# Optimization experiments

Measured on AMD Instinct MI355X. Metric: run time of the kernel, lower is better.

The kernel has to match this reference:

```python
import jax, jax.numpy as jnp
import numpy as np

B, NR, NF, NH, NFH, D, HID = 32, 32, 128, 64, 64, 32, 256


def setup_inputs() -> dict:
    key = jax.random.key(0)
    ks = jax.random.split(key, 16)

    def w(k, o, i):
        return (jax.random.normal(k, (o, i), jnp.float32) / np.sqrt(i)).astype(jnp.float32)

    inp = {
        "robot": jax.random.normal(ks[0], (B, NR, D), jnp.float32),
        "frontier": jax.random.normal(ks[1], (B, NF, D), jnp.float32),
        "robot_history": jax.random.normal(ks[2], (B, NH, D), jnp.float32),
        "frontier_history": jax.random.normal(ks[3], (B, NFH, D), jnp.float32),
        "robot_frontier": jax.random.uniform(ks[4], (B, NR, NF), jnp.float32),
        "robot_past": jax.random.uniform(ks[5], (B, NR, NH), jnp.float32),
        "frontier_past": jax.random.uniform(ks[6], (B, NF, NFH), jnp.float32),
        # parameters (torch Linear convention: weight [out, in])
        "Wq": w(ks[7], D, D), "bq": jnp.zeros(D, jnp.float32),
        "Wk": w(ks[8], D, D), "bk": jnp.zeros(D, jnp.float32),
        "Wv": w(ks[9], D, D), "bv": jnp.zeros(D, jnp.float32),
        "Wn1": w(ks[10], HID, 2 * D), "bn1": jnp.zeros(HID, jnp.float32),
        "Wn2": w(ks[11], D, HID), "bn2": jnp.zeros(D, jnp.float32),
        "We1": w(ks[12], HID, 2 * D + 1), "be1": jnp.zeros(HID, jnp.float32),
        "We2": w(ks[13], 1, HID), "be2": jnp.zeros(1, jnp.float32),
    }
    return inp


def reference(robot, frontier, robot_history, frontier_history, robot_frontier,
              robot_past, frontier_past, Wq, bq, Wk, bk, Wv, bv,
              Wn1, bn1, Wn2, bn2, We1, be1, We2, be2):
    def lin(x, W, b):
        return x @ W.T + b

    def nmlp(h):
        return lin(jax.nn.relu(lin(h, Wn1, bn1)), Wn2, bn2)

    def emlp(h):
        return lin(jax.nn.relu(lin(h, We1, be1)), We2, be2)

    def intra(x):  # x: [b, n, D]
        q, k, v = lin(x, Wq, bq), lin(x, Wk, bk), lin(x, Wv, bv)
        e = jax.nn.softmax(jnp.einsum('bnd,bmd->bnm', q, k), axis=-1)
        agg = jnp.einsum('bnm,bmd->bnd', e, v)
        return x + nmlp(jnp.concatenate([x, agg], axis=-1))

    def inter(x, y, dis):  # x: [b,Nx,D], y: [b,Ny,D], dis: [b,Nx,Ny]
        xq, yk, yv = lin(x, Wq, bq), lin(y, Wk, bk), lin(y, Wv, bv)
        b, Nx, _ = x.shape
        Ny = y.shape[1]
        r_i = jnp.broadcast_to(xq[:, :, None, :], (b, Nx, Ny, D))
        f_j = jnp.broadcast_to(yk[:, None, :, :], (b, Nx, Ny, D))
        edge_input = jnp.concatenate([r_i, f_j, dis[..., None]], axis=-1)  # [b,Nx,Ny,65]
        score = emlp(edge_input)[..., 0]                                   # [b,Nx,Ny]
        e = jax.nn.softmax(score, axis=-1)
        agg = jnp.einsum('bnm,bmd->bnd', e, yv)
        x = x + nmlp(jnp.concatenate([x, agg], axis=-1))
        return e, x

    robot = intra(robot)
    frontier = intra(frontier)           # == per-sample intra on [1,Nf,D]
    robot_history = intra(robot_history)
    frontier_history = intra(frontier_history)
    _, robot = inter(robot, robot_history, robot_past)
    _, new_frontier = inter(frontier, frontier_history, frontier_past)
    edge, robot = inter(robot, new_frontier, robot_frontier)
    # original returns the intra-transformed frontier (split_frontier), not new_frontier
    return (robot, frontier, robot_history, frontier_history, edge)
```

## Files before the change

### kernel.cpp

```cpp
#include <hip/hip_runtime.h>

#define BATCH 32
#define NRr 32
#define NFf 128
#define NHh 64
#define NFHh 64
#define TI 4

__device__ __forceinline__ float dot4(float4 a, float4 b) {
    return fmaf(a.x, b.x, fmaf(a.y, b.y, fmaf(a.z, b.z, a.w * b.w)));
}

__global__ __launch_bounds__(256, 4) void intra_kernel(
    const float* __restrict__ robot, const float* __restrict__ frontier,
    const float* __restrict__ rhist, const float* __restrict__ fhist,
    const float* __restrict__ Wq, const float* __restrict__ bq,
    const float* __restrict__ Wk, const float* __restrict__ bk,
    const float* __restrict__ Wv, const float* __restrict__ bv,
    const float* __restrict__ Wn1, const float* __restrict__ bn1,
    const float* __restrict__ Wn2, const float* __restrict__ bn2,
    float* __restrict__ o_robot, float* __restrict__ o_frontier,
    float* __restrict__ o_rh, float* __restrict__ o_fh)
{
    __shared__ __align__(16) float sXc[512];
    __shared__ __align__(16) float sQ[512];
    __shared__ __align__(16) float sQK[512];
    __shared__ __align__(16) float sAgg[512];
    __shared__ __align__(16) float sBig[6240];
    float* sS  = sBig;
    float* sXT = sBig + 2112;
    float* sT  = sBig;

    const int blk = blockIdx.x, tid = threadIdx.x;
    const float* xin; float* xout; int N, lgN, b, chunk;
    if (blk < 64)       { xin=robot;    xout=o_robot;    N=32;  lgN=5; b=blk>>1;       chunk=blk&1; }
    else if (blk < 320) { xin=frontier; xout=o_frontier; N=128; lgN=7; b=(blk-64)>>3;  chunk=(blk-64)&7; }
    else if (blk < 448) { xin=rhist;    xout=o_rh;       N=64;  lgN=6; b=(blk-320)>>2; chunk=(blk-320)&3; }
    else                { xin=fhist;    xout=o_fh;       N=64;  lgN=6; b=(blk-448)>>2; chunk=(blk-448)&3; }

    const int P = N + 4, P2 = N + 1;
    const float* xb = xin + (size_t)b * N * 32;
    const int r0 = chunk << 4;
    const int d = tid & 31;
    const int rloc = tid >> 5;

    sXc[tid] = xb[(r0 << 5) + tid];
    sXc[tid + 256] = xb[(r0 << 5) + tid + 256];
    for (int idx = tid; idx < (N << 5); idx += 256) {
        int j = idx >> 5, d2 = idx & 31;
        sXT[d2 * P2 + j] = xb[idx];
    }
    __syncthreads();

    {
        const float4* wq4 = (const float4*)(Wq + (d << 5));
        float4 wq[8];
        #pragma unroll
        for (int k = 0; k < 8; ++k) wq[k] = wq4[k];
        const float bqd = bq[d];
        #pragma unroll
        for (int p = 0; p < 2; ++p) {
            int rr = rloc + (p << 3);
            const float4* xr = (const float4*)(sXc + (rr << 5));
            float a = bqd;
            #pragma unroll
            for (int k = 0; k < 8; ++k) a += dot4(wq[k], xr[k]);
            sQ[(rr << 5) + d] = a;
        }
    }
    __syncthreads();

    {
        #pragma unroll
        for (int p = 0; p < 2; ++p) {
            int rr = rloc + (p << 3);
            const float* qr = sQ + (rr << 5);
            float a = 0.f;
            #pragma unroll
            for (int dd2 = 0; dd2 < 32; ++dd2)
                a = fmaf(Wk[dd2 * 32 + d], qr[dd2], a);
            sQK[(rr << 5) + d] = a;
        }
    }
    __syncthreads();

    for (int idx = tid; idx < (16 << lgN); idx += 256) {
        int r = idx >> lgN, j = idx & (N - 1);
        const float* qr = sQK + (r << 5);
        float a = 0.f;
        #pragma unroll
        for (int e = 0; e < 32; ++e) a = fmaf(qr[e], sXT[e * P2 + j], a);
        sS[r * P + j] = a;
    }
    __syncthreads();

    {
        #pragma unroll
        for (int p = 0; p < 2; ++p) {
            int rr = rloc + (p << 3);
            float* row = sS + rr * P;
            float m = -1e30f;
            for (int j = d; j < N; j += 32) m = fmaxf(m, row[j]);
            #pragma unroll
            for (int msk = 16; msk; msk >>= 1) m = fmaxf(m, __shfl_xor(m, msk));
            float s = 0.f;
            for (int j = d; j < N; j += 32) { float ev = __expf(row[j] - m); row[j] = ev; s += ev; }
            #pragma unroll
            for (int msk = 16; msk; msk >>= 1) s += __shfl_xor(s, msk);
            float inv = 1.0f / s;
            for (int j = d; j < N; j += 32) row[j] *= inv;
        }
    }
    __syncthreads();

    {
        #pragma unroll
        for (int p = 0; p < 2; ++p) {
            int rr = rloc + (p << 3);
            const float* er = sS + rr * P;
            const float* xtr = sXT + d * P2;
            float a = 0.f;
            for (int j = 0; j < N; ++j) a = fmaf(er[j], xtr[j], a);
            sQ[(rr << 5) + d] = a;
        }
    }
    __syncthreads();

    {
        const float4* wv4 = (const float4*)(Wv + (d << 5));
        float4 wv[8];
        #pragma unroll
        for (int k = 0; k < 8; ++k) wv[k] = wv4[k];
        const float bvd = bv[d];
        #pragma unroll
        for (int p = 0; p < 2; ++p) {
            int rr = rloc + (p << 3);
            const float4* zr = (const float4*)(sQ + (rr << 5));
            float a = bvd;
            #pragma unroll
            for (int k = 0; k < 8; ++k) a += dot4(wv[k], zr[k]);
            sAgg[(rr << 5) + d] = a;
        }
    }
    __syncthreads();

    {
        const float4* w14 = (const float4*)(Wn1 + (tid << 6));
        float4 w1r[16];
        #pragma unroll
        for (int k = 0; k < 16; ++k) w1r[k] = w14[k];
        const float b1 = bn1[tid];
        #pragma unroll
        for (int r = 0; r < 16; ++r) {
            const float4* xr = (const float4*)(sXc + (r << 5));
            const float4* ar = (const float4*)(sAgg + (r << 5));
            float a = b1;
            #pragma unroll
            for (int k = 0; k < 8; ++k) a += dot4(w1r[k], xr[k]);
            #pragma unroll
            for (int k = 0; k < 8; ++k) a += dot4(w1r[8 + k], ar[k]);
            sT[(r << 8) + tid] = fmaxf(a, 0.f);
        }
    }
    __syncthreads();

    {
        const int rg = tid >> 5;
        float acc0 = 0.f, acc1 = 0.f;
        #pragma unroll
        for (int hc = 0; hc < 4; ++hc) {
            const float4* w24 = (const float4*)(Wn2 + (d << 8) + (hc << 6));
            float4 w2r[16];
            #pragma unroll
            for (int k = 0; k < 16; ++k) w2r[k] = w24[k];
            const float4* t0 = (const float4*)(sT + (rg << 8) + (hc << 6));
            const float4* t1 = (const float4*)(sT + ((rg + 8) << 8) + (hc << 6));
            #pragma unroll
            for (int k = 0; k < 16; ++k) {
                acc0 += dot4(w2r[k], t0[k]);
                acc1 += dot4(w2r[k], t1[k]);
            }
        }
        const float b2 = bn2[d];
        const size_t base = ((size_t)b * N) << 5;
        xout[base + ((r0 + rg) << 5) + d]     = sXc[(rg << 5) + d] + b2 + acc0;
        xout[base + ((r0 + rg + 8) << 5) + d] = sXc[((rg + 8) << 5) + d] + b2 + acc1;
    }
}

__global__ __launch_bounds__(256) void pre_y_kernel(
    const float* __restrict__ yA, int NyA, float* __restrict__ wOutA, float* __restrict__ yvOutA, int nBlkA,
    const float* __restrict__ yB, int NyB, float* __restrict__ wOutB, float* __restrict__ yvOutB,
    int ghBase,
    const float* __restrict__ Wq, const float* __restrict__ bq,
    const float* __restrict__ Wk, const float* __restrict__ bk,
    const float* __restrict__ Wv, const float* __restrict__ bv,
    const float* __restrict__ We1, const float* __restrict__ be1,
    float* __restrict__ Gm, float* __restrict__ gvec,
    float* __restrict__ Hm, float* __restrict__ hbvec)
{
    __shared__ __align__(16) float sY[256], sK[256];
    const int blk = blockIdx.x, tid = threadIdx.x;

    if (blk >= ghBase) {
        const int hr = ((blk - ghBase) << 3) + (tid >> 5), e = tid & 31;
        const float* w1q = We1 + hr * 65;
        const float* w1k = w1q + 32;
        float aG = 0.f, aH = 0.f;
        #pragma unroll
        for (int d2 = 0; d2 < 32; ++d2) {
            aG = fmaf(w1q[d2], Wq[d2 * 32 + e], aG);
            aH = fmaf(w1k[d2], Wk[d2 * 32 + e], aH);
        }
        Gm[(hr << 5) + e] = aG;
        Hm[(hr << 5) + e] = aH;
        if (e == 0) {
            float ag = be1[hr], ahb = 0.f;
            #pragma unroll
            for (int d2 = 0; d2 < 32; ++d2) {
                ag  = fmaf(w1q[d2], bq[d2], ag);
                ahb = fmaf(w1k[d2], bk[d2], ahb);
            }
            gvec[hr] = ag;
            hbvec[hr] = ahb;
        }
        return;
    }

    const float* y; int Ny; float* wOut; float* yvOut; int idx;
    if (blk < nBlkA) { y=yA; Ny=NyA; wOut=wOutA; yvOut=yvOutA; idx=blk; }
    else             { y=yB; Ny=NyB; wOut=wOutB; yvOut=yvOutB; idx=blk-nBlkA; }
    const int chunks = Ny >> 3;
    const int b = idx / chunks, j0 = (idx - b * chunks) << 3;

    sY[tid] = y[((size_t)(b * Ny + j0)) * 32 + tid];
    __syncthreads();

    {
        int jl = tid >> 5, dd = tid & 31;
        const float4* wk4 = (const float4*)(Wk + (dd << 5));
        const float4* wv4 = (const float4*)(Wv + (dd << 5));
        const float4* yr = (const float4*)(sY + (jl << 5));
        float aK = bk[dd], aV = bv[dd];
        #pragma unroll
        for (int k = 0; k < 8; ++k) {
            float4 yv4 = yr[k];
            aK += dot4(wk4[k], yv4);
            aV += dot4(wv4[k], yv4);
        }
        sK[(jl << 5) + dd] = aK;
        yvOut[((size_t)(b * Ny + j0 + jl)) * 32 + dd] = aV;
    }
    __syncthreads();

    {
        const float* w1 = We1 + tid * 65 + 32;
        float acc[8] = {0,0,0,0,0,0,0,0};
        #pragma unroll
        for (int e = 0; e < 32; ++e) {
            float we = w1[e];
            #pragma unroll
            for (int jl = 0; jl < 8; ++jl)
                acc[jl] = fmaf(we, sK[(jl << 5) + e], acc[jl]);
        }
        float* wbase = wOut + (((size_t)b * 64 + (tid >> 2)) * Ny + j0) * 4 + (tid & 3);
        #pragma unroll
        for (int jl = 0; jl < 8; ++jl)
            wbase[jl << 2] = acc[jl];
    }
}

__global__ __launch_bounds__(256, 8) void inter_main_kernel(
    const float* __restrict__ xA, int NxA, const float* __restrict__ wA, const float* __restrict__ yvA,
    int NyA, const float* __restrict__ disA, float* __restrict__ outA, float* __restrict__ eA,
    float* __restrict__ wPreA, float* __restrict__ yvPreA, int nBlkA,
    const float* __restrict__ xB, int NxB, const float* __restrict__ wB, const float* __restrict__ yvB,
    int NyB, const float* __restrict__ disB, float* __restrict__ outB, float* __restrict__ eB,
    float* __restrict__ wPreB, float* __restrict__ yvPreB,
    const float* __restrict__ Gm, const float* __restrict__ gvec,
    const float* __restrict__ Hm, const float* __restrict__ hbvec,
    const float* __restrict__ Wv, const float* __restrict__ bv,
    const float* __restrict__ We1, const float* __restrict__ We2,
    const float* __restrict__ Wn1, const float* __restrict__ bn1,
    const float* __restrict__ Wn2, const float* __restrict__ bn2)
{
    __shared__ __align__(16) float sX[128];
    __shared__ __align__(16) float sQ[128];
    __shared__ __align__(16) float sAgg[128];
    __shared__ __align__(16) float sDis[512];
    __shared__ __align__(16) float sC[256];
    __shared__ __align__(16) float sW2[256];
    __shared__ __align__(16) float sS[512];
    __shared__ __align__(16) float sUT[1024];
    __shared__ __align__(16) float sPR[2048];

    const int blk = blockIdx.x, tid = threadIdx.x;
    const float* x; int Nx; const float* w; const float* yv; int Ny;
    const float* dis; float* outp; float* ep; float* wPre; float* yvPre; int idx;
    if (blk < nBlkA) { x=xA; Nx=NxA; w=wA; yv=yvA; Ny=NyA; dis=disA; outp=outA; ep=eA; wPre=wPreA; yvPre=yvPreA; idx=blk; }
    else             { x=xB; Nx=NxB; w=wB; yv=yvB; Ny=NyB; dis=disB; outp=outB; ep=eB; wPre=wPreB; yvPre=yvPreB; idx=blk-nBlkA; }
    const int lgNy = (Ny == 128) ? 7 : 6;
    const int tiles = Nx >> 2;
    const int b = idx / tiles, i0 = (idx - b * tiles) << 2;
    const float* xrow = x + ((size_t)(b * Nx + i0)) * 32;

    if (tid < 128) sX[tid] = xrow[tid];
    if (tid < Ny) {
        int il = tid >> (lgNy - 2), jq = tid & ((Ny >> 2) - 1);
        ((float4*)sDis)[(il << 5) + jq] =
            ((const float4*)(dis + ((size_t)(b * Nx + i0 + il)) * Ny))[jq];
    }
    __syncthreads();

    {
        const float* grow = Gm + (tid << 5);
        const float g0 = gvec[tid];
        float acc[TI];
        #pragma unroll
        for (int il = 0; il < TI; ++il) acc[il] = g0;
        #pragma unroll
        for (int e = 0; e < 32; ++e) {
            float we = grow[e];
            #pragma unroll
            for (int il = 0; il < TI; ++il)
                acc[il] = fmaf(we, sX[(il << 5) + e], acc[il]);
        }
        #pragma unroll
        for (int il = 0; il < TI; ++il) sUT[(il << 8) + tid] = acc[il];
        sC[tid] = We1[tid * 65 + 64];
        sW2[tid] = We2[tid];
    }
    __syncthreads();

    const int wv = tid >> 6, lane = tid & 63;
    {
        const int hc0 = wv << 4;
        const float4* wT4 = (const float4*)w + (size_t)(b * 64) * Ny;
        const float4* c4p = (const float4*)sC;
        const float4* p4p = (const float4*)sW2;
        if (Ny == 64) {
            float dv[TI];
            #pragma unroll
            for (int il = 0; il < TI; ++il) dv[il] = sDis[(il << 7) + lane];
            float acc[TI] = {0.f, 0.f, 0.f, 0.f};
            #pragma unroll
            for (int t = 0; t < 16; ++t) {
                int hc = hc0 + t;
                float4 w4 = wT4[((size_t)hc << 6) + lane];
                float4 c4 = c4p[hc], p4 = p4p[hc];
                #pragma unroll
                for (int il = 0; il < TI; ++il) {
                    float4 u4 = ((const float4*)(sUT + (il << 8)))[hc];
                    acc[il] = fmaf(p4.x, fmaxf(fmaf(c4.x, dv[il], u4.x + w4.x), 0.f), acc[il]);
                    acc[il] = fmaf(p4.y, fmaxf(fmaf(c4.y, dv[il], u4.y + w4.y), 0.f), acc[il]);
                    acc[il] = fmaf(p4.z, fmaxf(fmaf(c4.z, dv[il], u4.z + w4.z), 0.f), acc[il]);
                    acc[il] = fmaf(p4.w, fmaxf(fmaf(c4.w, dv[il], u4.w + w4.w), 0.f), acc[il]);
                }
            }
            #pragma unroll
            for (int il = 0; il < TI; ++il)
                sPR[(wv << 9) + (il << 7) + lane] = acc[il];
        } else {
            float dv0[TI], dv1[TI];
            #pragma unroll
            for (int il = 0; il < TI; ++il) {
                dv0[il] = sDis[(il << 7) + lane];
                dv1[il] = sDis[(il << 7) + 64 + lane];
            }
            float acc0[TI] = {0.f, 0.f, 0.f, 0.f};
            float acc1[TI] = {0.f, 0.f, 0.f, 0.f};
            #pragma unroll
            for (int t = 0; t < 16; ++t) {
                int hc = hc0 + t;
                float4 wa = wT4[((size_t)hc << 7) + lane];
                float4 wb = wT4[((size_t)hc << 7) + 64 + lane];
                float4 c4 = c4p[hc], p4 = p4p[hc];
                #pragma unroll
                for (int il = 0; il < TI; ++il) {
                    float4 u4 = ((const float4*)(sUT + (il << 8)))[hc];
                    acc0[il] = fmaf(p4.x, fmaxf(fmaf(c4.x, dv0[il], u4.x + wa.x), 0.f), acc0[il]);
                    acc0[il] = fmaf(p4.y, fmaxf(fmaf(c4.y, dv0[il], u4.y + wa.y), 0.f), acc0[il]);
                    acc0[il] = fmaf(p4.z, fmaxf(fmaf(c4.z, dv0[il], u4.z + wa.z), 0.f), acc0[il]);
                    acc0[il] = fmaf(p4.w, fmaxf(fmaf(c4.w, dv0[il], u4.w + wa.w), 0.f), acc0[il]);
                    acc1[il] = fmaf(p4.x, fmaxf(fmaf(c4.x, dv1[il], u4.x + wb.x), 0.f), acc1[il]);
                    acc1[il] = fmaf(p4.y, fmaxf(fmaf(c4.y, dv1[il], u4.y + wb.y), 0.f), acc1[il]);
                    acc1[il] = fmaf(p4.z, fmaxf(fmaf(c4.z, dv1[il], u4.z + wb.z), 0.f), acc1[il]);
                    acc1[il] = fmaf(p4.w, fmaxf(fmaf(c4.w, dv1[il], u4.w + wb.w), 0.f), acc1[il]);
                }
            }
            #pragma unroll
            for (int il = 0; il < TI; ++il) {
                sPR[(wv << 9) + (il << 7) + lane] = acc0[il];
                sPR[(wv << 9) + (il << 7) + 64 + lane] = acc1[il];
            }
        }
    }
    __syncthreads();

    {
        const int base = (wv << 7) + lane;
        float v0 = sPR[base] + sPR[512 + base] + sPR[1024 + base] + sPR[1536 + base];
        float v1 = -1e30f;
        if (Ny == 128) {
            const int b2 = base + 64;
            v1 = sPR[b2] + sPR[512 + b2] + sPR[1024 + b2] + sPR[1536 + b2];
        }
        float m = fmaxf(v0, v1);
        #pragma unroll
        for (int msk = 32; msk; msk >>= 1) m = fmaxf(m, __shfl_xor(m, msk));
        float e0 = __expf(v0 - m);
        float e1 = (Ny == 128) ? __expf(v1 - m) : 0.f;
        float s = e0 + e1;
        #pragma unroll
        for (int msk = 32; msk; msk >>= 1) s += __shfl_xor(s, msk);
        float inv = 1.0f / s;
        e0 *= inv; e1 *= inv;
        sS[base] = e0;
        if (Ny == 128) sS[base + 64] = e1;
        if (ep) {
            float* erow = ep + ((size_t)(b * Nx + i0 + wv)) * Ny;
            erow[lane] = e0;
            if (Ny == 128) erow[64 + lane] = e1;
        }
    }

    {
        const int dd = lane & 31, jg = lane >> 5;
        const float* yvg = yv + ((size_t)(b * Ny) << 5);
        float p = 0.f;
        #pragma unroll 8
        for (int j = jg; j < Ny; j += 2)
            p = fmaf(sS[(wv << 7) + j], yvg[(j << 5) + dd], p);
        p += __shfl_xor(p, 32);
        if (jg == 0) sAgg[(wv << 5) + dd] = p;
    }
    __syncthreads();

    {
        const float4* w14 = (const float4*)(Wn1 + (tid << 6));
        const float b1 = bn1[tid];
        float acc[TI];
        #pragma unroll
        for (int il = 0; il < TI; ++il) acc[il] = b1;
        #pragma unroll
        for (int k = 0; k < 8; ++k) {
            float4 wa = w14[k];
            #pragma unroll
            for (int il = 0; il < TI; ++il)
                acc[il] += dot4(wa, ((const float4*)(sX + (il << 5)))[k]);
        }
        #pragma unroll
        for (int k = 0; k < 8; ++k) {
            float4 wb = w14[8 + k];
            #pragma unroll
            for (int il = 0; il < TI; ++il)
                acc[il] += dot4(wb, ((const float4*)(sAgg + (il << 5)))[k]);
        }
        __syncthreads();
        #pragma unroll
        for (int il = 0; il < TI; ++il) sUT[(il << 8) + tid] = fmaxf(acc[il], 0.f);
    }
    __syncthreads();

    {
        const int hg = tid >> 5, dd = tid & 31;
        const float4* w24 = (const float4*)(Wn2 + (dd << 8) + (hg << 5));
        float4 w2r[8];
        #pragma unroll
        for (int k = 0; k < 8; ++k) w2r[k] = w24[k];
        float p[TI] = {0.f, 0.f, 0.f, 0.f};
        #pragma unroll
        for (int k = 0; k < 8; ++k) {
            #pragma unroll
            for (int il = 0; il < TI; ++il)
                p[il] += dot4(w2r[k], ((const float4*)(sUT + (il << 8) + (hg << 5)))[k]);
        }
        #pragma unroll
        for (int il = 0; il < TI; ++il) sPR[(hg << 7) + (il << 5) + dd] = p[il];
    }
    __syncthreads();
    if (tid < 128) {
        int il = tid >> 5, dd = tid & 31;
        float a = bn2[dd] + sX[tid];
        #pragma unroll
        for (int hg = 0; hg < 8; ++hg) a += sPR[(hg << 7) + tid];
        outp[((size_t)(b * Nx + i0 + il)) * 32 + dd] = a;
        if (wPre) sQ[tid] = a;
    }

    if (wPre) {
        __syncthreads();
        if (tid < 128) {
            int il = tid >> 5, dd = tid & 31;
            const float4* wm4 = (const float4*)(Wv + (dd << 5));
            const float4* orow = (const float4*)(sQ + (il << 5));
            float a = bv[dd];
            #pragma unroll
            for (int k = 0; k < 8; ++k) a += dot4(wm4[k], orow[k]);
            yvPre[(((size_t)(b * Nx + i0 + il)) << 5) + dd] = a;
        }
        {
            const float* hrow = Hm + (tid << 5);
            const float hb0 = hbvec[tid];
            float acc[4];
            #pragma unroll
            for (int il = 0; il < 4; ++il) acc[il] = hb0;
            #pragma unroll
            for (int e = 0; e < 32; ++e) {
                float we = hrow[e];
                #pragma unroll
                for (int il = 0; il < 4; ++il)
                    acc[il] = fmaf(we, sQ[(il << 5) + e], acc[il]);
            }
            float* wbase = wPre + (((size_t)b * 64 + (tid >> 2)) * Nx + i0) * 4 + (tid & 3);
            #pragma unroll
            for (int il = 0; il < 4; ++il)
                wbase[il << 2] = acc[il];
        }
    }
}

extern "C" void kernel_launch(void* const* d_in, const int* in_sizes, int n_in,
                              void* d_out, int out_size, void* d_ws, size_t ws_size,
                              hipStream_t stream) {
    const float* robot          = (const float*)d_in[0];
    const float* frontier       = (const float*)d_in[1];
    const float* rh             = (const float*)d_in[2];
    const float* fh             = (const float*)d_in[3];
    const float* robot_frontier = (const float*)d_in[4];
    const float* robot_past     = (const float*)d_in[5];
    const float* frontier_past  = (const float*)d_in[6];
    const float* Wq  = (const float*)d_in[7];  const float* bq  = (const float*)d_in[8];
    const float* Wk  = (const float*)d_in[9];  const float* bk  = (const float*)d_in[10];
    const float* Wv  = (const float*)d_in[11]; const float* bv  = (const float*)d_in[12];
    const float* Wn1 = (const float*)d_in[13]; const float* bn1 = (const float*)d_in[14];
    const float* Wn2 = (const float*)d_in[15]; const float* bn2 = (const float*)d_in[16];
    const float* We1 = (const float*)d_in[17]; const float* be1 = (const float*)d_in[18];
    const float* We2 = (const float*)d_in[19];

    float* out = (float*)d_out;
    float* out_robot    = out;
    float* out_frontier = out + 32768;
    float* out_rh       = out + 163840;
    float* out_fh       = out + 229376;
    float* out_edge     = out + 294912;

    float* W = (float*)d_ws;
    float* robot1 = W;
    float* robot2 = W + 32768;
    float* nf     = W + 65536;
    float* w5     = W + 196608;
    float* yv5    = W + 720896;
    float* w6     = W + 786432;
    float* yv6    = W + 1310720;
    float* w7     = W + 1376256;
    float* yv7    = W + 2424832;
    float* Gm     = W + 2555904;
    float* gvec   = W + 2564096;
    float* Hm     = W + 2564352;
    float* hbvec  = W + 2572544;

    intra_kernel<<<576, 256, 0, stream>>>(robot, frontier, rh, fh,
        Wq, bq, Wk, bk, Wv, bv, Wn1, bn1, Wn2, bn2,
        robot1, out_frontier, out_rh, out_fh);

    pre_y_kernel<<<544, 256, 0, stream>>>(
        out_rh, NHh, w5, yv5, BATCH * NHh / 8,
        out_fh, NFHh, w6, yv6,
        512,
        Wq, bq, Wk, bk, Wv, bv, We1, be1,
        Gm, gvec, Hm, hbvec);

    inter_main_kernel<<<1280, 256, 0, stream>>>(
        robot1, NRr, w5, yv5, NHh, robot_past, robot2,
        (float*)nullptr, (float*)nullptr, (float*)nullptr, BATCH * (NRr / TI),
        out_frontier, NFf, w6, yv6, NFHh, frontier_past, nf,
        (float*)nullptr, w7, yv7,
        Gm, gvec, Hm, hbvec, Wv, bv, We1, We2, Wn1, bn1, Wn2, bn2);

    inter_main_kernel<<<256, 256, 0, stream>>>(
        robot2, NRr, w7, yv7, NFf, robot_frontier, out_robot, out_edge,
        (float*)nullptr, (float*)nullptr, BATCH * (NRr / TI),
        robot2, NRr, w7, yv7, NFf, robot_frontier, out_robot, out_edge,
        (float*)nullptr, (float*)nullptr,
        Gm, gvec, Hm, hbvec, Wv, bv, We1, We2, Wn1, bn1, Wn2, bn2);
}
```

Measured before the change: 200.5 us.

## Fuse pre_y projections into intra kernel and remap block order for XCD locality

```diff
diff --git a/kernel.cpp b/kernel.cpp
--- a/kernel.cpp
+++ b/kernel.cpp
@@ -19,8 +19,13 @@
     const float* __restrict__ Wv, const float* __restrict__ bv,
     const float* __restrict__ Wn1, const float* __restrict__ bn1,
     const float* __restrict__ Wn2, const float* __restrict__ bn2,
+    const float* __restrict__ We1, const float* __restrict__ be1,
     float* __restrict__ o_robot, float* __restrict__ o_frontier,
-    float* __restrict__ o_rh, float* __restrict__ o_fh)
+    float* __restrict__ o_rh, float* __restrict__ o_fh,
+    float* __restrict__ w5, float* __restrict__ yv5,
+    float* __restrict__ w6, float* __restrict__ yv6,
+    float* __restrict__ Gm, float* __restrict__ gvec,
+    float* __restrict__ Hm, float* __restrict__ hbvec)
 {
     __shared__ __align__(16) float sXc[512];
     __shared__ __align__(16) float sQ[512];
@@ -31,12 +36,41 @@
     float* sXT = sBig + 2112;
     float* sT  = sBig;
 
-    const int blk = blockIdx.x, tid = threadIdx.x;
+    const int rawblk = blockIdx.x, tid = threadIdx.x;
+
+    if (rawblk >= 576) {
+        const int hr = ((rawblk - 576) << 3) + (tid >> 5), e = tid & 31;
+        const float* w1q = We1 + hr * 65;
+        const float* w1k = w1q + 32;
+        float aG = 0.f, aH = 0.f;
+        #pragma unroll
+        for (int d2 = 0; d2 < 32; ++d2) {
+            aG = fmaf(w1q[d2], Wq[d2 * 32 + e], aG);
+            aH = fmaf(w1k[d2], Wk[d2 * 32 + e], aH);
+        }
+        Gm[(hr << 5) + e] = aG;
+        Hm[(hr << 5) + e] = aH;
+        if (e == 0) {
+            float ag = be1[hr], ahb = 0.f;
+            #pragma unroll
+            for (int d2 = 0; d2 < 32; ++d2) {
+                ag  = fmaf(w1q[d2], bq[d2], ag);
+                ahb = fmaf(w1k[d2], bk[d2], ahb);
+            }
+            gvec[hr] = ag;
+            hbvec[hr] = ahb;
+        }
+        return;
+    }
+
+    const int blk = (rawblk & 7) * 72 + (rawblk >> 3);
+
     const float* xin; float* xout; int N, lgN, b, chunk;
+    float* wPre = nullptr; float* yvPre = nullptr;
     if (blk < 64)       { xin=robot;    xout=o_robot;    N=32;  lgN=5; b=blk>>1;       chunk=blk&1; }
     else if (blk < 320) { xin=frontier; xout=o_frontier; N=128; lgN=7; b=(blk-64)>>3;  chunk=(blk-64)&7; }
-    else if (blk < 448) { xin=rhist;    xout=o_rh;       N=64;  lgN=6; b=(blk-320)>>2; chunk=(blk-320)&3; }
-    else                { xin=fhist;    xout=o_fh;       N=64;  lgN=6; b=(blk-448)>>2; chunk=(blk-448)&3; }
+    else if (blk < 448) { xin=rhist;    xout=o_rh;       N=64;  lgN=6; b=(blk-320)>>2; chunk=(blk-320)&3; wPre=w5; yvPre=yv5; }
+    else                { xin=fhist;    xout=o_fh;       N=64;  lgN=6; b=(blk-448)>>2; chunk=(blk-448)&3; wPre=w6; yvPre=yv6; }
 
     const int P = N + 4, P2 = N + 1;
     const float* xb = xin + (size_t)b * N * 32;
@@ -183,90 +217,55 @@
         }
         const float b2 = bn2[d];
         const size_t base = ((size_t)b * N) << 5;
-        xout[base + ((r0 + rg) << 5) + d]     = sXc[(rg << 5) + d] + b2 + acc0;
-        xout[base + ((r0 + rg + 8) << 5) + d] = sXc[((rg + 8) << 5) + d] + b2 + acc1;
-    }
-}
-
-__global__ __launch_bounds__(256) void pre_y_kernel(
-    const float* __restrict__ yA, int NyA, float* __restrict__ wOutA, float* __restrict__ yvOutA, int nBlkA,
-    const float* __restrict__ yB, int NyB, float* __restrict__ wOutB, float* __restrict__ yvOutB,
-    int ghBase,
-    const float* __restrict__ Wq, const float* __restrict__ bq,
-    const float* __restrict__ Wk, const float* __restrict__ bk,
-    const float* __restrict__ Wv, const float* __restrict__ bv,
-    const float* __restrict__ We1, const float* __restrict__ be1,
-    float* __restrict__ Gm, float* __restrict__ gvec,
-    float* __restrict__ Hm, float* __restrict__ hbvec)
-{
-    __shared__ __align__(16) float sY[256], sK[256];
-    const int blk = blockIdx.x, tid = threadIdx.x;
-
-    if (blk >= ghBase) {
-        const int hr = ((blk - ghBase) << 3) + (tid >> 5), e = tid & 31;
-        const float* w1q = We1 + hr * 65;
-        const float* w1k = w1q + 32;
-        float aG = 0.f, aH = 0.f;
-        #pragma unroll
-        for (int d2 = 0; d2 < 32; ++d2) {
-            aG = fmaf(w1q[d2], Wq[d2 * 32 + e], aG);
-            aH = fmaf(w1k[d2], Wk[d2 * 32 + e], aH);
-        }
-        Gm[(hr << 5) + e] = aG;
-        Hm[(hr << 5) + e] = aH;
-        if (e == 0) {
-            float ag = be1[hr], ahb = 0.f;
-            #pragma unroll
-            for (int d2 = 0; d2 < 32; ++d2) {
-                ag  = fmaf(w1q[d2], bq[d2], ag);
-                ahb = fmaf(w1k[d2], bk[d2], ahb);
-            }
-            gvec[hr] = ag;
-            hbvec[hr] = ahb;
-        }
-        return;
-    }
-
-    const float* y; int Ny; float* wOut; float* yvOut; int idx;
-    if (blk < nBlkA) { y=yA; Ny=NyA; wOut=wOutA; yvOut=yvOutA; idx=blk; }
-    else             { y=yB; Ny=NyB; wOut=wOutB; yvOut=yvOutB; idx=blk-nBlkA; }
-    const int chunks = Ny >> 3;
-    const int b = idx / chunks, j0 = (idx - b * chunks) << 3;
-
-    sY[tid] = y[((size_t)(b * Ny + j0)) * 32 + tid];
-    __syncthreads();
-
-    {
-        int jl = tid >> 5, dd = tid & 31;
-        const float4* wk4 = (const float4*)(Wk + (dd << 5));
-        const float4* wv4 = (const float4*)(Wv + (dd << 5));
-        const float4* yr = (const float4*)(sY + (jl << 5));
-        float aK = bk[dd], aV = bv[dd];
-        #pragma unroll
-        for (int k = 0; k < 8; ++k) {
-            float4 yv4 = yr[k];
-            aK += dot4(wk4[k], yv4);
-            aV += dot4(wv4[k], yv4);
-        }
-        sK[(jl << 5) + dd] = aK;
-        yvOut[((size_t)(b * Ny + j0 + jl)) * 32 + dd] = aV;
-    }
-    __syncthreads();
-
-    {
-        const float* w1 = We1 + tid * 65 + 32;
-        float acc[8] = {0,0,0,0,0,0,0,0};
-        #pragma unroll
-        for (int e = 0; e < 32; ++e) {
-            float we = w1[e];
-            #pragma unroll
-            for (int jl = 0; jl < 8; ++jl)
-                acc[jl] = fmaf(we, sK[(jl << 5) + e], acc[jl]);
-        }
-        float* wbase = wOut + (((size_t)b * 64 + (tid >> 2)) * Ny + j0) * 4 + (tid & 3);
-        #pragma unroll
-        for (int jl = 0; jl < 8; ++jl)
-            wbase[jl << 2] = acc[jl];
+        float o0 = sXc[(rg << 5) + d] + b2 + acc0;
+        float o1 = sXc[((rg + 8) << 5) + d] + b2 + acc1;
+        xout[base + ((r0 + rg) << 5) + d]     = o0;
+        xout[base + ((r0 + rg + 8) << 5) + d] = o1;
+        if (wPre) {
+            sQ[(rg << 5) + d] = o0;
+            sQ[((rg + 8) << 5) + d] = o1;
+        }
+    }
+
+    if (wPre) {
+        __syncthreads();
+        {
+            const float4* wk4 = (const float4*)(Wk + (d << 5));
+            const float4* wv4 = (const float4*)(Wv + (d << 5));
+            const float bkd = bk[d], bvd = bv[d];
+            #pragma unroll
+            for (int p = 0; p < 2; ++p) {
+                int rr = rloc + (p << 3);
+                const float4* orow = (const float4*)(sQ + (rr << 5));
+                float aK = bkd, aV = bvd;
+                #pragma unroll
+                for (int k = 0; k < 8; ++k) {
+                    float4 o = orow[k];
+                    aK += dot4(wk4[k], o);
+                    aV += dot4(wv4[k], o);
+                }
+                sQK[(rr << 5) + d] = aK;
+                yvPre[((size_t)(b * N + r0 + rr) << 5) + d] = aV;
+            }
+        }
+        __syncthreads();
+        {
+            const float* w1 = We1 + tid * 65 + 32;
+            float acc[16];
+            #pragma unroll
+            for (int jl = 0; jl < 16; ++jl) acc[jl] = 0.f;
+            #pragma unroll
+            for (int e = 0; e < 32; ++e) {
+                float we = w1[e];
+                #pragma unroll
+                for (int jl = 0; jl < 16; ++jl)
+                    acc[jl] = fmaf(we, sQK[(jl << 5) + e], acc[jl]);
+            }
+            float* wbase = wPre + (((size_t)b * 64 + (tid >> 2)) * N + r0) * 4 + (tid & 3);
+            #pragma unroll
+            for (int jl = 0; jl < 16; ++jl)
+                wbase[jl << 2] = acc[jl];
+        }
     }
 }
 
@@ -294,7 +293,10 @@
     __shared__ __align__(16) float sUT[1024];
     __shared__ __align__(16) float sPR[2048];
 
-    const int blk = blockIdx.x, tid = threadIdx.x;
+    const int tid = threadIdx.x;
+    const int chunkx = (int)gridDim.x >> 3;
+    const int blk = ((int)blockIdx.x & 7) * chunkx + ((int)blockIdx.x >> 3);
+
     const float* x; int Nx; const float* w; const float* yv; int Ny;
     const float* dis; float* outp; float* ep; float* wPre; float* yvPre; int idx;
     if (blk < nBlkA) { x=xA; Nx=NxA; w=wA; yv=yvA; Ny=NyA; dis=disA; outp=outA; ep=eA; wPre=wPreA; yvPre=yvPreA; idx=blk; }
@@ -560,16 +562,10 @@
     float* Hm     = W + 2564352;
     float* hbvec  = W + 2572544;
 
-    intra_kernel<<<576, 256, 0, stream>>>(robot, frontier, rh, fh,
-        Wq, bq, Wk, bk, Wv, bv, Wn1, bn1, Wn2, bn2,
-        robot1, out_frontier, out_rh, out_fh);
-
-    pre_y_kernel<<<544, 256, 0, stream>>>(
-        out_rh, NHh, w5, yv5, BATCH * NHh / 8,
-        out_fh, NFHh, w6, yv6,
-        512,
-        Wq, bq, Wk, bk, Wv, bv, We1, be1,
-        Gm, gvec, Hm, hbvec);
+    intra_kernel<<<608, 256, 0, stream>>>(robot, frontier, rh, fh,
+        Wq, bq, Wk, bk, Wv, bv, Wn1, bn1, Wn2, bn2, We1, be1,
+        robot1, out_frontier, out_rh, out_fh,
+        w5, yv5, w6, yv6, Gm, gvec, Hm, hbvec);
 
     inter_main_kernel<<<1280, 256, 0, stream>>>(
         robot1, NRr, w5, yv5, NHh, robot_past, robot2,
```

After: 223.5 us. 1.11x slower.
